# Kernel optimization log

Hardware: AMD Instinct MI355X
Metric: run time of the kernel (lower is better)

## Reference

```python
import jax, jax.numpy as jnp
import numpy as np

N, F, H, F_ = 8192, 256, 2, 64
NEG_MASK = -1e10
LEAKY_SLOPE = 0.2


def setup_inputs() -> dict:
    key = jax.random.key(0)
    k0, k1, k2, k3 = jax.random.split(key, 4)
    X = jax.random.normal(k0, (N, F), jnp.float32)
    A = (jax.random.uniform(k1, (N, N)) < 0.01).astype(jnp.float32)
    A = jnp.maximum(A, jnp.eye(N, dtype=jnp.float32))
    W = jax.random.normal(k2, (H, F, F_), jnp.float32) * (1.0 / np.sqrt(F))
    b = jnp.zeros((H, F_), jnp.float32)
    a = jax.random.normal(k3, (H, F_), jnp.float32) * 0.1
    return {"X": X, "A": A, "W": W, "b": b, "a": a}


def reference(X, A, W, b, a):
    # per-head projected features: [H, N, F_]
    feats = jnp.einsum('nf,hfo->hno', X, W)
    # score[h,i,j] = sum_o feats[h,i,o] * feats[h,j,o] * a[h,o]
    # (identical math to Dot(axes=-1)([X_0*X_1, a^T]) without the [N,N,F_] tensor)
    scores = jnp.einsum('hno,hmo->hnm', feats * a[:, None, :], feats)
    scores = jax.nn.leaky_relu(scores, negative_slope=LEAKY_SLOPE)
    scores = scores + NEG_MASK * (1.0 - A)  # adjacency mask (broadcast over heads)
    attn = jax.nn.softmax(scores, axis=-1)  # [H, N, N]
    # dropout_rate=0 -> identity at inference
    out = jnp.einsum('hnm,hmo->hno', attn, feats) + b[:, None, :]  # [H, N, F_]
    out = jnp.transpose(out, (1, 0, 2)).reshape(X.shape[0], H * F_)  # concat heads
    return jax.nn.relu(out)
```

## Files before the change

kernel.cpp:

```cpp
#include <hip/hip_runtime.h>

#define NN 8192
#define FIN 256
#define FO 64
#define CAP 192

__global__ __launch_bounds__(256) void feats_kernel(
    const float* __restrict__ X,
    const float* __restrict__ W,
    float* __restrict__ feats)
{
    __shared__ float Ws[128*FO];
    __shared__ float Xs[32*132];
    const int h = blockIdx.y;
    const int row0 = blockIdx.x * 32;
    const int t = threadIdx.x;
    const int rg = t >> 4;
    const int c0 = (t & 15) << 2;
    float acc0[4] = {0.f,0.f,0.f,0.f};
    float acc1[4] = {0.f,0.f,0.f,0.f};

    for (int kp = 0; kp < 2; ++kp){
        const int kb = kp * 128;
        const float* Wh = W + h*FIN*FO + kb*FO;
        #pragma unroll
        for (int it=0; it<8; ++it){
            int flat = (it*256 + t)*4;
            *(float4*)&Ws[flat] = *(const float4*)&Wh[flat];
        }
        #pragma unroll
        for (int it=0; it<4; ++it){
            int flat = (it*256 + t)*4;
            int r = flat >> 7, f0 = flat & 127;
            *(float4*)&Xs[r*132 + f0] = *(const float4*)&X[(size_t)(row0+r)*FIN + kb + f0];
        }
        __syncthreads();
        const float* xp0 = &Xs[(rg*2+0)*132];
        const float* xp1 = &Xs[(rg*2+1)*132];
        #pragma unroll 4
        for (int k=0; k<128; ++k){
            float x0 = xp0[k], x1 = xp1[k];
            float4 w4 = *(const float4*)&Ws[k*FO + c0];
            acc0[0]=fmaf(x0,w4.x,acc0[0]); acc0[1]=fmaf(x0,w4.y,acc0[1]);
            acc0[2]=fmaf(x0,w4.z,acc0[2]); acc0[3]=fmaf(x0,w4.w,acc0[3]);
            acc1[0]=fmaf(x1,w4.x,acc1[0]); acc1[1]=fmaf(x1,w4.y,acc1[1]);
            acc1[2]=fmaf(x1,w4.z,acc1[2]); acc1[3]=fmaf(x1,w4.w,acc1[3]);
        }
        __syncthreads();
    }
    float* o0 = feats + ((size_t)(row0 + rg*2 + 0)*2 + h)*FO + c0;
    float* o1 = feats + ((size_t)(row0 + rg*2 + 1)*2 + h)*FO + c0;
    *(float4*)o0 = make_float4(acc0[0],acc0[1],acc0[2],acc0[3]);
    *(float4*)o1 = make_float4(acc1[0],acc1[1],acc1[2],acc1[3]);
}

__global__ __launch_bounds__(256) void csr_kernel(
    const float* __restrict__ A,
    int* __restrict__ cnt,
    int* __restrict__ nbr)
{
    __shared__ int s_n[CAP];
    __shared__ int s_c;
    const int i = blockIdx.x, t = threadIdx.x;
    const int w = t >> 6, l = t & 63;
    if (t == 0) s_c = 0;
    __syncthreads();

    const float4* Arow = (const float4*)(A + (size_t)i*NN + w*2048);
    float4 v[8];
    #pragma unroll
    for (int it=0; it<8; ++it) v[it] = Arow[it*64 + l];

    const unsigned long long ltmask = (1ull << l) - 1ull;
    #pragma unroll
    for (int it=0; it<8; ++it){
        int colb = w*2048 + it*256 + l*4;
        float vals[4] = {v[it].x, v[it].y, v[it].z, v[it].w};
        #pragma unroll
        for (int e=0; e<4; ++e){
            bool nz = (vals[e] != 0.0f);
            unsigned long long m = __ballot(nz);
            int base = 0;
            if (l == 0) base = atomicAdd(&s_c, __popcll(m));
            base = __shfl(base, 0, 64);
            if (nz){
                int p = base + __popcll(m & ltmask);
                if (p < CAP) s_n[p] = colb + e;
            }
        }
    }
    __syncthreads();
    int n = min(s_c, CAP);
    if (t == 0) cnt[i] = n;
    for (int k=t; k<n; k+=256) nbr[(size_t)i*CAP + k] = s_n[k];
}

__global__ __launch_bounds__(256) void attn_kernel(
    const float* __restrict__ feats,
    const float* __restrict__ av,
    const float* __restrict__ bv,
    const int* __restrict__ cnt,
    const int* __restrict__ nbr,
    float* __restrict__ out)
{
    __shared__ float fls[64*132];
    __shared__ int   nbrl[CAP];
    __shared__ float ssh[2][64];
    __shared__ float psh[2][64];
    __shared__ float bc[4];
    __shared__ float part[4*128];

    const int i = blockIdx.x, t = threadIdx.x;
    const int lane32 = t & 31;
    const int nbloc  = t >> 5;
    const int gag    = t >> 6;
    const int op     = t & 63;

    float4 qa = *(const float4*)&av[lane32*4];
    float4 qf = *(const float4*)&feats[(size_t)i*128 + lane32*4];
    float4 q4 = make_float4(qf.x*qa.x, qf.y*qa.y, qf.z*qa.z, qf.w*qa.w);

    const int n = cnt[i];
    for (int k=t; k<n; k+=256) nbrl[k] = nbr[(size_t)i*CAP + k];
    __syncthreads();

    float m0 = -1e30f, m1 = -1e30f, l0 = 0.f, l1 = 0.f;
    float2 acc = make_float2(0.f, 0.f);
    const int nch = (n + 63) >> 6;

    for (int c=0; c<nch; ++c){
        const int base = c*64;
        const int nv = min(n - base, 64);

        #pragma unroll
        for (int it=0; it<8; ++it){
            int kk = it*8 + nbloc;
            int j = (kk < nv) ? nbrl[base + kk] : i;
            float4 f4 = *(const float4*)&feats[(size_t)j*128 + lane32*4];
            *(float4*)&fls[kk*132 + lane32*4] = f4;
            float d = f4.x*q4.x + f4.y*q4.y + f4.z*q4.z + f4.w*q4.w;
            d += __shfl_xor(d, 1, 64);
            d += __shfl_xor(d, 2, 64);
            d += __shfl_xor(d, 4, 64);
            d += __shfl_xor(d, 8, 64);
            if (lane32 == 0)  ssh[0][kk] = (kk < nv) ? d : -1e30f;
            if (lane32 == 16) ssh[1][kk] = (kk < nv) ? d : -1e30f;
        }
        __syncthreads();

        if (t < 64){
            float s0 = ssh[0][t]; s0 = (s0 >= 0.f) ? s0 : 0.2f*s0;
            float s1 = ssh[1][t]; s1 = (s1 >= 0.f) ? s1 : 0.2f*s1;
            float cm0 = s0, cm1 = s1;
            #pragma unroll
            for (int off=32; off; off>>=1){
                cm0 = fmaxf(cm0, __shfl_xor(cm0, off, 64));
                cm1 = fmaxf(cm1, __shfl_xor(cm1, off, 64));
            }
            float nm0 = fmaxf(m0, cm0), nm1 = fmaxf(m1, cm1);
            float al0 = __expf(m0 - nm0), al1 = __expf(m1 - nm1);
            float p0 = __expf(s0 - nm0), p1 = __expf(s1 - nm1);
            psh[0][t] = p0; psh[1][t] = p1;
            float sp0 = p0, sp1 = p1;
            #pragma unroll
            for (int off=32; off; off>>=1){
                sp0 += __shfl_xor(sp0, off, 64);
                sp1 += __shfl_xor(sp1, off, 64);
            }
            l0 = l0*al0 + sp0; l1 = l1*al1 + sp1;
            m0 = nm0; m1 = nm1;
            if (t == 0){ bc[0] = al0; bc[1] = al1; }
        }
        __syncthreads();

        const float alph = bc[op >> 5];
        const float* pr = psh[op >> 5];
        acc.x *= alph; acc.y *= alph;
        for (int k=gag; k<nv; k+=4){
            float p = pr[k];
            float2 f2 = *(const float2*)&fls[k*132 + op*2];
            acc.x = fmaf(p, f2.x, acc.x);
            acc.y = fmaf(p, f2.y, acc.y);
        }
        __syncthreads();
    }

    if (t == 0){ bc[2] = l0; bc[3] = l1; }
    *(float2*)&part[gag*128 + op*2] = acc;
    __syncthreads();

    if (t < 128){
        int o = t, h = o >> 6;
        float s = part[o] + part[128+o] + part[256+o] + part[384+o];
        float val = s / bc[2+h] + bv[o];
        out[(size_t)i*128 + o] = fmaxf(val, 0.f);
    }
}

extern "C" void kernel_launch(void* const* d_in, const int* in_sizes, int n_in,
                              void* d_out, int out_size, void* d_ws, size_t ws_size,
                              hipStream_t stream) {
    const float* X = (const float*)d_in[0];
    const float* A = (const float*)d_in[1];
    const float* W = (const float*)d_in[2];
    const float* b = (const float*)d_in[3];
    const float* a = (const float*)d_in[4];
    float* out = (float*)d_out;

    char* ws = (char*)d_ws;
    float* feats = (float*)ws;
    int*   cnt   = (int*)(ws + (size_t)NN*2*FO*4);
    int*   nbrs  = (int*)(ws + (size_t)NN*2*FO*4 + NN*4);

    feats_kernel<<<dim3(NN/32, 2), 256, 0, stream>>>(X, W, feats);
    csr_kernel  <<<dim3(NN),       256, 0, stream>>>(A, cnt, nbrs);
    attn_kernel <<<dim3(NN),       256, 0, stream>>>(feats, a, b, cnt, nbrs, out);
}
```

Measured before the change: 469.8 us.

## Fuse CSR extraction and sparse attention into one per-row kernel

Merges the adjacency compaction kernel and the attention kernel into a single 512-thread kernel per row. Neighbor indices stay in shared memory instead of round-tripping through global workspace. The online chunked softmax is replaced by a two-pass max/sum over all neighbor scores held in shared memory. The aggregation now reads neighbor features from global memory again rather than from a staged shared tile, so the second feature pass relies on cache hits.

```diff
diff --git a/kernel.cpp b/kernel.cpp
--- a/kernel.cpp
+++ b/kernel.cpp
@@ -54,28 +54,40 @@
     *(float4*)o1 = make_float4(acc1[0],acc1[1],acc1[2],acc1[3]);
 }
 
-__global__ __launch_bounds__(256) void csr_kernel(
+__global__ __launch_bounds__(512) void gat_kernel(
     const float* __restrict__ A,
-    int* __restrict__ cnt,
-    int* __restrict__ nbr)
+    const float* __restrict__ feats,
+    const float* __restrict__ av,
+    const float* __restrict__ bv,
+    float* __restrict__ out)
 {
-    __shared__ int s_n[CAP];
-    __shared__ int s_c;
+    __shared__ int   nsh[CAP];
+    __shared__ float s0[CAP], s1[CAP];
+    __shared__ float part[4*128];
+    __shared__ float red[2];
+    __shared__ int   s_c;
+
     const int i = blockIdx.x, t = threadIdx.x;
-    const int w = t >> 6, l = t & 63;
+    const int l  = t & 63;
+    const int wv = t >> 6;
+    const int gi = t >> 5, l32 = t & 31;
+
+    float4 qa = *(const float4*)&av[l32*4];
+    float4 qf = *(const float4*)&feats[(size_t)i*128 + l32*4];
+    const float4 q4 = make_float4(qf.x*qa.x, qf.y*qa.y, qf.z*qa.z, qf.w*qa.w);
+
     if (t == 0) s_c = 0;
     __syncthreads();
 
-    const float4* Arow = (const float4*)(A + (size_t)i*NN + w*2048);
-    float4 v[8];
+    const float4* Arow4 = (const float4*)(A + (size_t)i*NN);
+    float4 v[4];
     #pragma unroll
-    for (int it=0; it<8; ++it) v[it] = Arow[it*64 + l];
+    for (int r=0; r<4; ++r) v[r] = Arow4[r*512 + t];
 
     const unsigned long long ltmask = (1ull << l) - 1ull;
     #pragma unroll
-    for (int it=0; it<8; ++it){
-        int colb = w*2048 + it*256 + l*4;
-        float vals[4] = {v[it].x, v[it].y, v[it].z, v[it].w};
+    for (int r=0; r<4; ++r){
+        float vals[4] = {v[r].x, v[r].y, v[r].z, v[r].w};
         #pragma unroll
         for (int e=0; e<4; ++e){
             bool nz = (vals[e] != 0.0f);
@@ -85,115 +97,55 @@
             base = __shfl(base, 0, 64);
             if (nz){
                 int p = base + __popcll(m & ltmask);
-                if (p < CAP) s_n[p] = colb + e;
+                if (p < CAP) nsh[p] = (r*512 + t)*4 + e;
             }
         }
     }
     __syncthreads();
-    int n = min(s_c, CAP);
-    if (t == 0) cnt[i] = n;
-    for (int k=t; k<n; k+=256) nbr[(size_t)i*CAP + k] = s_n[k];
-}
+    const int n = min(s_c, CAP);
 
-__global__ __launch_bounds__(256) void attn_kernel(
-    const float* __restrict__ feats,
-    const float* __restrict__ av,
-    const float* __restrict__ bv,
-    const int* __restrict__ cnt,
-    const int* __restrict__ nbr,
-    float* __restrict__ out)
-{
-    __shared__ float fls[64*132];
-    __shared__ int   nbrl[CAP];
-    __shared__ float ssh[2][64];
-    __shared__ float psh[2][64];
-    __shared__ float bc[4];
-    __shared__ float part[4*128];
-
-    const int i = blockIdx.x, t = threadIdx.x;
-    const int lane32 = t & 31;
-    const int nbloc  = t >> 5;
-    const int gag    = t >> 6;
-    const int op     = t & 63;
-
-    float4 qa = *(const float4*)&av[lane32*4];
-    float4 qf = *(const float4*)&feats[(size_t)i*128 + lane32*4];
-    float4 q4 = make_float4(qf.x*qa.x, qf.y*qa.y, qf.z*qa.z, qf.w*qa.w);
-
-    const int n = cnt[i];
-    for (int k=t; k<n; k+=256) nbrl[k] = nbr[(size_t)i*CAP + k];
+    for (int k=gi; k<n; k+=16){
+        int j = nsh[k];
+        float4 f4 = *(const float4*)&feats[(size_t)j*128 + l32*4];
+        float d = f4.x*q4.x + f4.y*q4.y + f4.z*q4.z + f4.w*q4.w;
+        d += __shfl_xor(d, 1, 64);
+        d += __shfl_xor(d, 2, 64);
+        d += __shfl_xor(d, 4, 64);
+        d += __shfl_xor(d, 8, 64);
+        d = (d >= 0.f) ? d : 0.2f*d;
+        if (l32 == 0)  s0[k] = d;
+        if (l32 == 16) s1[k] = d;
+    }
     __syncthreads();
 
-    float m0 = -1e30f, m1 = -1e30f, l0 = 0.f, l1 = 0.f;
-    float2 acc = make_float2(0.f, 0.f);
-    const int nch = (n + 63) >> 6;
+    if (wv < 2){
+        float* ss = wv ? s1 : s0;
+        float m = -1e30f;
+        for (int k=l; k<n; k+=64) m = fmaxf(m, ss[k]);
+        #pragma unroll
+        for (int off=32; off; off>>=1) m = fmaxf(m, __shfl_xor(m, off, 64));
+        float sum = 0.f;
+        for (int k=l; k<n; k+=64){ float p = __expf(ss[k]-m); ss[k] = p; sum += p; }
+        #pragma unroll
+        for (int off=32; off; off>>=1) sum += __shfl_xor(sum, off, 64);
+        if (l == 0) red[wv] = sum;
+    }
+    __syncthreads();
 
-    for (int c=0; c<nch; ++c){
-        const int base = c*64;
-        const int nv = min(n - base, 64);
-
-        #pragma unroll
-        for (int it=0; it<8; ++it){
-            int kk = it*8 + nbloc;
-            int j = (kk < nv) ? nbrl[base + kk] : i;
-            float4 f4 = *(const float4*)&feats[(size_t)j*128 + lane32*4];
-            *(float4*)&fls[kk*132 + lane32*4] = f4;
-            float d = f4.x*q4.x + f4.y*q4.y + f4.z*q4.z + f4.w*q4.w;
-            d += __shfl_xor(d, 1, 64);
-            d += __shfl_xor(d, 2, 64);
-            d += __shfl_xor(d, 4, 64);
-            d += __shfl_xor(d, 8, 64);
-            if (lane32 == 0)  ssh[0][kk] = (kk < nv) ? d : -1e30f;
-            if (lane32 == 16) ssh[1][kk] = (kk < nv) ? d : -1e30f;
-        }
-        __syncthreads();
-
-        if (t < 64){
-            float s0 = ssh[0][t]; s0 = (s0 >= 0.f) ? s0 : 0.2f*s0;
-            float s1 = ssh[1][t]; s1 = (s1 >= 0.f) ? s1 : 0.2f*s1;
-            float cm0 = s0, cm1 = s1;
-            #pragma unroll
-            for (int off=32; off; off>>=1){
-                cm0 = fmaxf(cm0, __shfl_xor(cm0, off, 64));
-                cm1 = fmaxf(cm1, __shfl_xor(cm1, off, 64));
-            }
-            float nm0 = fmaxf(m0, cm0), nm1 = fmaxf(m1, cm1);
-            float al0 = __expf(m0 - nm0), al1 = __expf(m1 - nm1);
-            float p0 = __expf(s0 - nm0), p1 = __expf(s1 - nm1);
-            psh[0][t] = p0; psh[1][t] = p1;
-            float sp0 = p0, sp1 = p1;
-            #pragma unroll
-            for (int off=32; off; off>>=1){
-                sp0 += __shfl_xor(sp0, off, 64);
-                sp1 += __shfl_xor(sp1, off, 64);
-            }
-            l0 = l0*al0 + sp0; l1 = l1*al1 + sp1;
-            m0 = nm0; m1 = nm1;
-            if (t == 0){ bc[0] = al0; bc[1] = al1; }
-        }
-        __syncthreads();
-
-        const float alph = bc[op >> 5];
-        const float* pr = psh[op >> 5];
-        acc.x *= alph; acc.y *= alph;
-        for (int k=gag; k<nv; k+=4){
-            float p = pr[k];
-            float2 f2 = *(const float2*)&fls[k*132 + op*2];
-            acc.x = fmaf(p, f2.x, acc.x);
-            acc.y = fmaf(p, f2.y, acc.y);
-        }
-        __syncthreads();
+    const int op = t & 127, g = t >> 7;
+    const float* ps = (op >= 64) ? s1 : s0;
+    float acc = 0.f;
+    for (int k=g; k<n; k+=4){
+        int j = nsh[k];
+        acc = fmaf(ps[k], feats[(size_t)j*128 + op], acc);
     }
-
-    if (t == 0){ bc[2] = l0; bc[3] = l1; }
-    *(float2*)&part[gag*128 + op*2] = acc;
+    part[g*128 + op] = acc;
     __syncthreads();
 
     if (t < 128){
-        int o = t, h = o >> 6;
-        float s = part[o] + part[128+o] + part[256+o] + part[384+o];
-        float val = s / bc[2+h] + bv[o];
-        out[(size_t)i*128 + o] = fmaxf(val, 0.f);
+        float num = part[t] + part[128+t] + part[256+t] + part[384+t];
+        float val = num / red[t>>6] + bv[t];
+        out[(size_t)i*128 + t] = fmaxf(val, 0.f);
     }
 }
 
@@ -207,12 +159,8 @@
     const float* a = (const float*)d_in[4];
     float* out = (float*)d_out;
 
-    char* ws = (char*)d_ws;
-    float* feats = (float*)ws;
-    int*   cnt   = (int*)(ws + (size_t)NN*2*FO*4);
-    int*   nbrs  = (int*)(ws + (size_t)NN*2*FO*4 + NN*4);
+    float* feats = (float*)d_ws;
 
     feats_kernel<<<dim3(NN/32, 2), 256, 0, stream>>>(X, W, feats);
-    csr_kernel  <<<dim3(NN),       256, 0, stream>>>(A, cnt, nbrs);
-    attn_kernel <<<dim3(NN),       256, 0, stream>>>(feats, a, b, cnt, nbrs, out);
+    gat_kernel  <<<dim3(NN),       512, 0, stream>>>(A, feats, a, b, out);
 }
```

Result: faster. 428.5 us (-8.8%).
